# Performance work log

Measured on AMD Instinct MI355X. Metric: run time of the kernel, lower is better.

Reference implementation:

```python
import jax, jax.numpy as jnp
import numpy as np

NUM_GROUPS = 32
EPS = 1e-6


def group_norm(x, gamma, beta):
    # x: [b, c, h, w]
    b, c, h, w = x.shape
    g = NUM_GROUPS
    xg = x.reshape(b, g, c // g, h, w)
    mean = jnp.mean(xg, axis=(2, 3, 4), keepdims=True)
    var = jnp.var(xg, axis=(2, 3, 4), keepdims=True)
    xg = (xg - mean) * jax.lax.rsqrt(var + EPS)
    x = xg.reshape(b, c, h, w)
    return x * gamma[None, :, None, None] + beta[None, :, None, None]


def conv1x1(x, w, bias):
    # x: [b, c_in, h, w], w: [c_out, c_in], bias: [c_out]
    return jnp.einsum('bihw,oi->bohw', x, w) + bias[None, :, None, None]


def setup_inputs() -> dict:
    key = jax.random.key(0)
    ks = jax.random.split(key, 10)
    c = 512
    b, h, w = 4, 64, 64
    scale = 1.0 / np.sqrt(c)
    inp = {
        'x': jax.random.normal(ks[0], (b, c, h, w), dtype=jnp.float32),
        'gn_gamma': jnp.ones((c,), dtype=jnp.float32),
        'gn_beta': jnp.zeros((c,), dtype=jnp.float32),
        'wq': jax.random.normal(ks[1], (c, c), dtype=jnp.float32) * scale,
        'bq': jnp.zeros((c,), dtype=jnp.float32),
        'wk': jax.random.normal(ks[2], (c, c), dtype=jnp.float32) * scale,
        'bk': jnp.zeros((c,), dtype=jnp.float32),
        'wv': jax.random.normal(ks[3], (c, c), dtype=jnp.float32) * scale,
        'bv': jnp.zeros((c,), dtype=jnp.float32),
        'wo': jax.random.normal(ks[4], (c, c), dtype=jnp.float32) * scale,
        'bo': jnp.zeros((c,), dtype=jnp.float32),
    }
    return inp


def reference(x, gn_gamma, gn_beta, wq, bq, wk, bk, wv, bv, wo, bo):
    b, c, h, w = x.shape
    h_ = group_norm(x, gn_gamma, gn_beta)
    q = conv1x1(h_, wq, bq)
    k = conv1x1(h_, wk, bk)
    v = conv1x1(h_, wv, bv)
    n = h * w
    q = q.reshape(b, c, n).transpose(0, 2, 1)  # [b, n, c]
    k = k.reshape(b, c, n)                      # [b, c, n]
    v = v.reshape(b, c, n).transpose(0, 2, 1)  # [b, n, c]
    sim = jnp.einsum('bqc,bck->bqk', q, k) * (c ** -0.5)  # [b, n, n]
    attn = jax.nn.softmax(sim, axis=-1)
    out = jnp.einsum('bqk,bkc->bqc', attn, v)  # [b, n, c]
    out = out.transpose(0, 2, 1).reshape(b, c, h, w)
    out = conv1x1(out, wo, bo)
    return x + out
```

## Files before the change

### kernel.cpp

```cpp
#include <hip/hip_runtime.h>


typedef __attribute__((ext_vector_type(8))) short bf16x8;
typedef __attribute__((ext_vector_type(4))) float f32x4;

#define MFMA16(a, b, c) __builtin_amdgcn_mfma_f32_16x16x32_bf16((a), (b), (c), 0, 0, 0)

#define B_   4
#define C_   512
#define N_   4096
#define SCALE 0.044194173824159216f
#define ESHIFT 12.0f

__device__ __forceinline__ unsigned short f2bf(float f) {
    union { float f; unsigned int u; } v; v.f = f;
    unsigned int r = (v.u + 0x7fffu + ((v.u >> 16) & 1u)) >> 16;
    return (unsigned short)r;
}
__device__ __forceinline__ float bf2f(unsigned short s) {
    union { unsigned int u; float f; } v; v.u = ((unsigned int)s) << 16;
    return v.f;
}

__device__ __forceinline__ void async16(const unsigned short* g, unsigned short* l) {
    __builtin_amdgcn_global_load_lds((const __attribute__((address_space(1))) unsigned int*)g,
                                     (__attribute__((address_space(3))) unsigned int*)l,
                                     16, 0, 0);
}

__global__ __launch_bounds__(256) void gn_partial(const float* __restrict__ x,
                                                  float* __restrict__ part) {
    int blk = blockIdx.x;
    int gid = blk >> 2, qtr = blk & 3;
    const float4* base = (const float4*)(x + (size_t)gid * 65536) + qtr * 4096;
    float s = 0.f, ss = 0.f;
    for (int i = threadIdx.x; i < 4096; i += 256) {
        float4 v = base[i];
        s  += v.x + v.y + v.z + v.w;
        ss += v.x * v.x + v.y * v.y + v.z * v.z + v.w * v.w;
    }
    __shared__ float red[512];
    int t = threadIdx.x;
    red[t] = s; red[256 + t] = ss;
    __syncthreads();
    for (int st = 128; st > 0; st >>= 1) {
        if (t < st) { red[t] += red[t + st]; red[256 + t] += red[256 + t + st]; }
        __syncthreads();
    }
    if (t == 0) { part[blk] = red[0]; part[512 + blk] = red[256]; }
}

__global__ __launch_bounds__(256) void gn_apply(const float* __restrict__ x,
                                                const float* __restrict__ gamma,
                                                const float* __restrict__ beta,
                                                const float* __restrict__ part,
                                                unsigned short* __restrict__ ht) {
    __shared__ float tile[64][65];
    __shared__ float mrs[4][2];
    int j0 = blockIdx.x * 64, c0 = blockIdx.y * 64, b = blockIdx.z;
    int t = threadIdx.x;
    if (t < 4) {
        int gid = b * 32 + (c0 >> 4) + t;
        float s = 0.f, ss = 0.f;
#pragma unroll
        for (int q = 0; q < 4; ++q) { s += part[gid * 4 + q]; ss += part[512 + gid * 4 + q]; }
        float mean = s * (1.f / 65536.f);
        float var  = ss * (1.f / 65536.f) - mean * mean;
        mrs[t][0] = mean;
        mrs[t][1] = rsqrtf(var + 1e-6f);
    }
    __syncthreads();
#pragma unroll
    for (int i = 0; i < 16; ++i) {
        int lid = i * 256 + t;
        int cl = lid >> 6, jl = lid & 63;
        int c = c0 + cl;
        float v = x[((size_t)b * C_ + c) * N_ + j0 + jl];
        tile[cl][jl] = (v - mrs[cl >> 4][0]) * mrs[cl >> 4][1] * gamma[c] + beta[c];
    }
    __syncthreads();
#pragma unroll
    for (int i = 0; i < 16; ++i) {
        int lid = i * 256 + t;
        int jl = lid >> 6, cl = lid & 63;
        ht[((size_t)b * N_ + j0 + jl) * C_ + c0 + cl] = f2bf(tile[cl][jl]);
    }
}

__global__ __launch_bounds__(256) void wconv(const float* __restrict__ wq,
                                             const float* __restrict__ wk,
                                             const float* __restrict__ wv,
                                             const float* __restrict__ wo,
                                             unsigned short* __restrict__ dst) {
    size_t i = (size_t)blockIdx.x * 256 + threadIdx.x;
    int m = (int)(i >> 18);
    size_t off = i & 262143;
    const float* src = (m == 0) ? wq : (m == 1) ? wk : (m == 2) ? wv : wo;
    dst[i] = f2bf(src[off]);
}

template <typename EPI>
__device__ __forceinline__ void gemm_core(const unsigned short* __restrict__ Abase,
                                          const unsigned short* __restrict__ Bbase,
                                          size_t lda, size_t ldb, int K, EPI epi) {
    __shared__ unsigned short hl[2][128 * 64];
    __shared__ unsigned short wl[2][128 * 64];
    int t = threadIdx.x;
    int wv = t >> 6, lane = t & 63, l15 = lane & 15, quad = lane >> 4;
    int wm = wv & 1, wn = wv >> 1;
    int srow = lane >> 3;
    int sch  = ((lane & 7) ^ srow) * 8;
    int xr = l15 & 7;
    f32x4 acc[4][4] = {};
#pragma unroll
    for (int i = 0; i < 4; ++i) {
        int seg = wv * 4 + i;
        size_t row = seg * 8 + srow;
        async16(&Abase[row * lda + sch], &hl[0][seg * 512]);
        async16(&Bbase[row * ldb + sch], &wl[0][seg * 512]);
    }
    int nk = K >> 6;
    for (int k = 0; k < nk; ++k) {
        int cur = k & 1;
        __builtin_amdgcn_s_waitcnt(0x3F70);
        __syncthreads();
        if (k + 1 < nk) {
            int k0 = (k + 1) << 6;
#pragma unroll
            for (int i = 0; i < 4; ++i) {
                int seg = wv * 4 + i;
                size_t row = seg * 8 + srow;
                async16(&Abase[row * lda + k0 + sch], &hl[cur ^ 1][seg * 512]);
                async16(&Bbase[row * ldb + k0 + sch], &wl[cur ^ 1][seg * 512]);
            }
        }
#pragma unroll
        for (int kk = 0; kk < 2; ++kk) {
            int sl = (((kk << 2) + quad) ^ xr) * 8;
            bf16x8 af[4], bfr[4];
#pragma unroll
            for (int mi = 0; mi < 4; ++mi)
                af[mi] = *(const bf16x8*)&hl[cur][(wm * 64 + mi * 16 + l15) * 64 + sl];
#pragma unroll
            for (int ni = 0; ni < 4; ++ni)
                bfr[ni] = *(const bf16x8*)&wl[cur][(wn * 64 + ni * 16 + l15) * 64 + sl];
#pragma unroll
            for (int mi = 0; mi < 4; ++mi)
#pragma unroll
                for (int ni = 0; ni < 4; ++ni)
                    acc[mi][ni] = MFMA16(af[mi], bfr[ni], acc[mi][ni]);
        }
    }
    epi(acc, wm, wn, l15, quad);
}

__global__ __launch_bounds__(256) void gemm_qkv(const unsigned short* __restrict__ Ht,
                                                const unsigned short* __restrict__ Wb,
                                                const float* __restrict__ bq,
                                                const float* __restrict__ bk,
                                                const float* __restrict__ bv,
                                                unsigned short* __restrict__ Qt,
                                                unsigned short* __restrict__ Kt,
                                                unsigned short* __restrict__ Vg) {
    int b = blockIdx.z, j0 = blockIdx.x * 128;
    int ct = blockIdx.y;
    int slab = ct >> 2, co0 = (ct & 3) * 128;
    const unsigned short* A = Ht + ((size_t)b * N_ + j0) * C_;
    const unsigned short* B = Wb + (size_t)slab * C_ * C_ + (size_t)co0 * C_;
    const float* bias = (slab == 0) ? bq : (slab == 1) ? bk : bv;
    unsigned short* outqk = (slab == 0) ? Qt : Kt;
    gemm_core(A, B, C_, C_, C_,
        [&](f32x4 (&acc)[4][4], int wm, int wn, int l15, int quad) {
        if (slab < 2) {
#pragma unroll
            for (int mi = 0; mi < 4; ++mi)
#pragma unroll
                for (int ni = 0; ni < 4; ++ni)
#pragma unroll
                    for (int r = 0; r < 4; ++r) {
                        int mrow = wm * 64 + mi * 16 + quad * 4 + r;
                        int ncol = wn * 64 + ni * 16 + l15;
                        outqk[((size_t)b * N_ + j0 + mrow) * C_ + co0 + ncol] =
                            f2bf(acc[mi][ni][r] + bias[co0 + ncol]);
                    }
        } else {
#pragma unroll
            for (int mi = 0; mi < 4; ++mi)
#pragma unroll
                for (int ni = 0; ni < 4; ++ni) {
                    int ncol = wn * 64 + ni * 16 + l15;
                    float bb = bias[co0 + ncol];
                    ushort4 pk;
                    pk.x = f2bf(acc[mi][ni][0] + bb);
                    pk.y = f2bf(acc[mi][ni][1] + bb);
                    pk.z = f2bf(acc[mi][ni][2] + bb);
                    pk.w = f2bf(acc[mi][ni][3] + bb);
                    int jb = j0 + wm * 64 + mi * 16 + quad * 4;
                    *(ushort4*)&Vg[((size_t)b * C_ + co0 + ncol) * N_ + jb] = pk;
                }
        }
    });
}

__global__ __launch_bounds__(512, 2) void gemm_qk_exp(const unsigned short* __restrict__ Qt,
                                                      const unsigned short* __restrict__ Kt,
                                                      unsigned short* __restrict__ P,
                                                      float* __restrict__ psum) {
    extern __shared__ unsigned short sm[];
    int b = blockIdx.z, j0 = blockIdx.x * 256, ky = blockIdx.y;
    int kc0 = ky * 256;
    const unsigned short* A  = Qt + ((size_t)b * N_ + j0) * C_;
    const unsigned short* Bm = Kt + ((size_t)b * N_ + kc0) * C_;

    int t = threadIdx.x;
    int w = t >> 6, lane = t & 63, l15 = lane & 15, quad = lane >> 4;
    int wm = w >> 2, wn = w & 3;
    int srow = lane >> 2;
    int sch  = (((lane & 3) ^ ((lane >> 3) & 3))) * 8;
    int slotq = (quad ^ ((l15 >> 1) & 3)) * 8;

    f32x4 acc[8][4] = {};

    const int NT = 16;
#pragma unroll
    for (int tt = 0; tt < 3; ++tt) {
        unsigned short* dst = sm + (tt << 14);
        size_t k0 = (size_t)tt << 5;
#pragma unroll
        for (int i = 0; i < 2; ++i) {
            int seg = w * 2 + i;
            size_t row = (size_t)seg * 16 + srow;
            async16(&A [row * C_ + k0 + sch], dst + seg * 512);
            async16(&Bm[row * C_ + k0 + sch], dst + 8192 + seg * 512);
        }
    }
    __builtin_amdgcn_s_waitcnt(0x3F78);
    __builtin_amdgcn_s_barrier();

    for (int tt = 0; tt < NT; ++tt) {
        const unsigned short* bp = sm + ((tt & 3) << 14);
        unsigned short* stg = sm + (((tt + 3) & 3) << 14);
        const bool dostage = (tt + 3 < NT);
        size_t k0n = (size_t)(tt + 3) << 5;
        bf16x8 bfr[4], af[4];
#pragma unroll
        for (int ni = 0; ni < 4; ++ni)
            bfr[ni] = *(const bf16x8*)&bp[8192 + (wn * 64 + ni * 16 + l15) * 32 + slotq];
#pragma unroll
        for (int mi = 0; mi < 4; ++mi)
            af[mi] = *(const bf16x8*)&bp[(wm * 128 + mi * 16 + l15) * 32 + slotq];
        if (dostage) {
#pragma unroll
            for (int i = 0; i < 2; ++i) {
                int seg = w * 2 + i;
                size_t row = (size_t)seg * 16 + srow;
                async16(&A[row * C_ + k0n + sch], stg + seg * 512);
            }
        }
        __builtin_amdgcn_s_barrier();
        __builtin_amdgcn_s_setprio(1);
#pragma unroll
        for (int mi = 0; mi < 4; ++mi)
#pragma unroll
            for (int ni = 0; ni < 4; ++ni)
                acc[mi][ni] = MFMA16(af[mi], bfr[ni], acc[mi][ni]);
        __builtin_amdgcn_s_setprio(0);
        __builtin_amdgcn_s_barrier();
#pragma unroll
        for (int mi = 0; mi < 4; ++mi)
            af[mi] = *(const bf16x8*)&bp[(wm * 128 + (mi + 4) * 16 + l15) * 32 + slotq];
        if (dostage) {
#pragma unroll
            for (int i = 0; i < 2; ++i) {
                int seg = w * 2 + i;
                size_t row = (size_t)seg * 16 + srow;
                async16(&Bm[row * C_ + k0n + sch], stg + 8192 + seg * 512);
            }
        }
        __builtin_amdgcn_s_barrier();
        __builtin_amdgcn_s_setprio(1);
#pragma unroll
        for (int mi = 0; mi < 4; ++mi)
#pragma unroll
            for (int ni = 0; ni < 4; ++ni)
                acc[4 + mi][ni] = MFMA16(af[mi], bfr[ni], acc[4 + mi][ni]);
        __builtin_amdgcn_s_setprio(0);
        if (tt + 1 < NT) {
            if (tt < NT - 3)       __builtin_amdgcn_s_waitcnt(0x3F78);
            else if (tt == NT - 3) __builtin_amdgcn_s_waitcnt(0x3F74);
            else                   __builtin_amdgcn_s_waitcnt(0x3F70);
            __builtin_amdgcn_s_barrier();
        }
    }

#pragma unroll
    for (int mi = 0; mi < 8; ++mi) {
        float rs[4] = {0.f, 0.f, 0.f, 0.f};
#pragma unroll
        for (int ni = 0; ni < 4; ++ni) {
            int ncol = kc0 + wn * 64 + ni * 16 + l15;
#pragma unroll
            for (int r = 0; r < 4; ++r) {
                int mrow = j0 + wm * 128 + mi * 16 + quad * 4 + r;
                float p = __expf(acc[mi][ni][r] * SCALE - ESHIFT);
                rs[r] += p;
                P[((size_t)b * N_ + mrow) * N_ + ncol] = f2bf(p);
            }
        }
#pragma unroll
        for (int r = 0; r < 4; ++r) {
            float v = rs[r];
            v += __shfl_xor(v, 1);
            v += __shfl_xor(v, 2);
            v += __shfl_xor(v, 4);
            v += __shfl_xor(v, 8);
            if (l15 == 0)
                psum[(size_t)(wn * 16 + ky) * 16384 +
                     (size_t)b * N_ + j0 + wm * 128 + mi * 16 + quad * 4 + r] = v;
        }
    }
}

__global__ __launch_bounds__(256) void gemm_pv(const unsigned short* __restrict__ P,
                                               const unsigned short* __restrict__ Vg,
                                               const float* __restrict__ psum,
                                               unsigned short* __restrict__ ao) {
    __shared__ float linv[128];
    int flat = blockIdx.x;
    int xcd = flat & 7, rr = flat >> 3;
    int ct = rr & 3, g = (rr >> 2) * 8 + xcd;
    int b = g & 3, qtile = g >> 2;
    int j0 = qtile * 128, co0 = ct * 128;
    int t = threadIdx.x;
    if (t < 128) {
        size_t q = (size_t)b * N_ + j0 + t;
        float s = 0.f;
#pragma unroll
        for (int i = 0; i < 64; ++i) s += psum[(size_t)i * 16384 + q];
        linv[t] = 1.f / s;
    }
    const unsigned short* A = P + ((size_t)b * N_ + j0) * N_;
    const unsigned short* B = Vg + ((size_t)b * C_ + co0) * N_;
    gemm_core(A, B, N_, N_, N_,
        [&](f32x4 (&acc)[4][4], int wm, int wn, int l15, int quad) {
#pragma unroll
        for (int mi = 0; mi < 4; ++mi)
#pragma unroll
            for (int ni = 0; ni < 4; ++ni)
#pragma unroll
                for (int r = 0; r < 4; ++r) {
                    int mrow = wm * 64 + mi * 16 + quad * 4 + r;
                    int ncol = wn * 64 + ni * 16 + l15;
                    ao[((size_t)b * N_ + j0 + mrow) * C_ + co0 + ncol] =
                        f2bf(acc[mi][ni][r] * linv[mrow]);
                }
    });
}

__global__ __launch_bounds__(256) void gemm_resid(const unsigned short* __restrict__ AObf,
                                                  const unsigned short* __restrict__ Wo,
                                                  const float* __restrict__ bo,
                                                  const float* __restrict__ xres,
                                                  float* __restrict__ out) {
    int b = blockIdx.z, j0 = blockIdx.x * 128, co0 = blockIdx.y * 128;
    const unsigned short* A = AObf + ((size_t)b * N_ + j0) * C_;
    const unsigned short* B = Wo + (size_t)co0 * C_;
    gemm_core(A, B, C_, C_, C_,
        [&](f32x4 (&acc)[4][4], int wm, int wn, int l15, int quad) {
#pragma unroll
        for (int mi = 0; mi < 4; ++mi)
#pragma unroll
            for (int ni = 0; ni < 4; ++ni) {
                int ncol = wn * 64 + ni * 16 + l15;
                int jb = j0 + wm * 64 + mi * 16 + quad * 4;
                size_t o = ((size_t)b * C_ + co0 + ncol) * N_ + jb;
                float bb = bo[co0 + ncol];
                float4 xr = *(const float4*)&xres[o];
                float4 ov;
                ov.x = acc[mi][ni][0] + bb + xr.x;
                ov.y = acc[mi][ni][1] + bb + xr.y;
                ov.z = acc[mi][ni][2] + bb + xr.z;
                ov.w = acc[mi][ni][3] + bb + xr.w;
                *(float4*)&out[o] = ov;
            }
    });
}

__global__ __launch_bounds__(256, 1) void flash_attn(const unsigned short* __restrict__ Qt,
                                                     const unsigned short* __restrict__ Kt,
                                                     const unsigned short* __restrict__ Vg,
                                                     unsigned short* __restrict__ part,
                                                     float* __restrict__ lbuf,
                                                     int nsplit) {
    extern __shared__ unsigned short smem[];
    unsigned short* Kl = smem;
    unsigned short* Vl = smem + 32768;
    unsigned short* Pl = smem + 65536;

    int flat = blockIdx.x;
    int qblk, b, s;
    if (nsplit == 2) { s = flat & 1; b = (flat >> 1) & 3; qblk = flat >> 3; }
    else             { s = 0;        b = flat & 3;        qblk = flat >> 2; }
    int q0 = qblk * 128;
    int t = threadIdx.x, w = t >> 6, lane = t & 63, l15 = lane & 15, quad = lane >> 4;
    int klen = N_ / nsplit, kbeg = s * klen, nkt = klen / 32;
    int xr = l15 & 7;

    const unsigned short* Kbase = Kt + (size_t)b * N_ * C_;
    const unsigned short* Vbase = Vg + (size_t)b * C_ * N_;

    bf16x8 qa[2][16];
#pragma unroll
    for (int u = 0; u < 2; ++u) {
        const unsigned short* qb =
            Qt + ((size_t)b * N_ + q0 + w * 32 + u * 16 + l15) * C_ + quad * 8;
#pragma unroll
        for (int ck = 0; ck < 16; ++ck) qa[u][ck] = *(const bf16x8*)(qb + ck * 32);
    }

    f32x4 o[2][32] = {};
    float lrow[2][4] = {};

    {
        int k0 = kbeg;
#pragma unroll
        for (int i = 0; i < 8; ++i) {
            int r = w * 8 + i;
            async16(Kbase + (size_t)(k0 + r) * C_ + ((lane ^ (r & 7)) * 8), Kl + r * 512);
        }
#pragma unroll
        for (int i = 0; i < 8; ++i) {
            int idx = w * 8 + i, kc = idx >> 3, cb = idx & 7;
            async16(Vbase + (size_t)(cb * 64 + lane) * N_ + k0 + kc * 8,
                    Vl + (kc * 512 + cb * 64) * 8);
        }
    }

    for (int kt = 0; kt < nkt; ++kt) {
        int cur = kt & 1, nxt = cur ^ 1;
        __builtin_amdgcn_s_waitcnt(0x3F70);
        __syncthreads();
        if (kt + 1 < nkt) {
            int k0 = kbeg + (kt + 1) * 32;
#pragma unroll
            for (int i = 0; i < 8; ++i) {
                int r = w * 8 + i;
                async16(Kbase + (size_t)(k0 + r) * C_ + ((lane ^ (r & 7)) * 8),
                        Kl + nxt * 16384 + r * 512);
            }
#pragma unroll
            for (int i = 0; i < 8; ++i) {
                int idx = w * 8 + i, kc = idx >> 3, cb = idx & 7;
                async16(Vbase + (size_t)(cb * 64 + lane) * N_ + k0 + kc * 8,
                        Vl + nxt * 16384 + (kc * 512 + cb * 64) * 8);
            }
        }
        const unsigned short* Kc = Kl + cur * 16384;
        f32x4 s00 = {}, s01 = {}, s10 = {}, s11 = {};
#pragma unroll
        for (int ck = 0; ck < 16; ++ck) {
            int slot = (ck * 4 + quad) ^ xr;
            bf16x8 b0 = *(const bf16x8*)&Kc[l15 * 512 + slot * 8];
            bf16x8 b1 = *(const bf16x8*)&Kc[(16 + l15) * 512 + slot * 8];
            s00 = MFMA16(qa[0][ck], b0, s00);
            s10 = MFMA16(qa[1][ck], b0, s10);
            s01 = MFMA16(qa[0][ck], b1, s01);
            s11 = MFMA16(qa[1][ck], b1, s11);
        }
        unsigned short* pb = &Pl[w * 1152];
#pragma unroll
        for (int r = 0; r < 4; ++r) {
            float p00 = __expf(s00[r] * SCALE - ESHIFT);
            float p01 = __expf(s01[r] * SCALE - ESHIFT);
            float p10 = __expf(s10[r] * SCALE - ESHIFT);
            float p11 = __expf(s11[r] * SCALE - ESHIFT);
            lrow[0][r] += p00 + p01;
            lrow[1][r] += p10 + p11;
            int row0 = (quad * 4 + r) * 36;
            int row1 = (16 + quad * 4 + r) * 36;
            pb[row0 + l15]      = f2bf(p00);
            pb[row0 + 16 + l15] = f2bf(p01);
            pb[row1 + l15]      = f2bf(p10);
            pb[row1 + 16 + l15] = f2bf(p11);
        }
        __builtin_amdgcn_s_waitcnt(0xC07F);
        bf16x8 pa0 = *(const bf16x8*)&Pl[w * 1152 + l15 * 36 + quad * 8];
        bf16x8 pa1 = *(const bf16x8*)&Pl[w * 1152 + (16 + l15) * 36 + quad * 8];
        const unsigned short* Vc = Vl + cur * 16384;
#pragma unroll
        for (int cf = 0; cf < 32; ++cf) {
            bf16x8 vb = *(const bf16x8*)&Vc[(quad * 512 + cf * 16 + l15) * 8];
            o[0][cf] = MFMA16(pa0, vb, o[0][cf]);
            o[1][cf] = MFMA16(pa1, vb, o[1][cf]);
        }
    }
#pragma unroll
    for (int u = 0; u < 2; ++u)
#pragma unroll
        for (int r = 0; r < 4; ++r) {
            float l = lrow[u][r];
            l += __shfl_xor(l, 1);
            l += __shfl_xor(l, 2);
            l += __shfl_xor(l, 4);
            l += __shfl_xor(l, 8);
            lrow[u][r] = l;
        }
    size_t pbase = (size_t)(s * B_ + b) * N_;
#pragma unroll
    for (int u = 0; u < 2; ++u)
#pragma unroll
        for (int cf = 0; cf < 32; ++cf)
#pragma unroll
            for (int r = 0; r < 4; ++r) {
                int q = q0 + w * 32 + u * 16 + quad * 4 + r;
                part[(pbase + q) * C_ + cf * 16 + l15] = f2bf(o[u][cf][r]);
            }
    if (l15 == 0) {
#pragma unroll
        for (int u = 0; u < 2; ++u)
#pragma unroll
            for (int r = 0; r < 4; ++r) {
                int q = q0 + w * 32 + u * 16 + quad * 4 + r;
                lbuf[pbase + q] = lrow[u][r];
            }
    }
}

__global__ __launch_bounds__(256) void attn_combine(const unsigned short* __restrict__ part,
                                                    const float* __restrict__ lbuf,
                                                    unsigned short* __restrict__ ao,
                                                    int nsplit) {
    size_t idx = (size_t)blockIdx.x * 256 + threadIdx.x;
    int cu = (int)(idx & 63);
    size_t row = idx >> 6;
    float l = lbuf[row];
    union { uint4 v; unsigned short u[8]; } p1, p2, outv;
    p1.v = *(const uint4*)&part[row * C_ + cu * 8];
    if (nsplit == 2) {
        l += lbuf[(size_t)B_ * N_ + row];
        p2.v = *(const uint4*)&part[((size_t)B_ * N_ + row) * C_ + cu * 8];
    } else {
        p2.v = make_uint4(0, 0, 0, 0);
    }
    float inv = 1.f / l;
#pragma unroll
    for (int j = 0; j < 8; ++j)
        outv.u[j] = f2bf((bf2f(p1.u[j]) + bf2f(p2.u[j])) * inv);
    *(uint4*)&ao[row * C_ + cu * 8] = outv.v;
}

extern "C" void kernel_launch(void* const* d_in, const int* in_sizes, int n_in,
                              void* d_out, int out_size, void* d_ws, size_t ws_size,
                              hipStream_t stream) {
    const float* x   = (const float*)d_in[0];
    const float* gam = (const float*)d_in[1];
    const float* bet = (const float*)d_in[2];
    const float* wq  = (const float*)d_in[3];
    const float* bq  = (const float*)d_in[4];
    const float* wk  = (const float*)d_in[5];
    const float* bk  = (const float*)d_in[6];
    const float* wv  = (const float*)d_in[7];
    const float* bv  = (const float*)d_in[8];
    const float* wo  = (const float*)d_in[9];
    const float* bo  = (const float*)d_in[10];
    float* out = (float*)d_out;

    char* ws = (char*)d_ws;
    const size_t SZH = (size_t)B_ * N_ * C_ * 2;
    const size_t OFF_HT = 4096;
    const size_t OFF_QT = OFF_HT + SZH;
    const size_t OFF_KT = OFF_QT + SZH;
    const size_t OFF_VG = OFF_KT + SZH;
    const size_t OFF_WB = OFF_VG + SZH;
    const size_t OFF_X  = OFF_WB + 2097152;
    float*          part0 = (float*)ws;
    unsigned short* Ht    = (unsigned short*)(ws + OFF_HT);
    unsigned short* Qt    = (unsigned short*)(ws + OFF_QT);
    unsigned short* Kt    = (unsigned short*)(ws + OFF_KT);
    unsigned short* Vg    = (unsigned short*)(ws + OFF_VG);
    unsigned short* Wb    = (unsigned short*)(ws + OFF_WB);
    unsigned short* AObf  = Ht;

    const size_t SZPSUM = 64ull * 16384 * 4;
    const size_t SZP    = (size_t)B_ * N_ * N_ * 2;
    float*          psum = (float*)(ws + OFF_X);
    unsigned short* P    = (unsigned short*)(ws + OFF_X + SZPSUM);
    size_t needA = OFF_X + SZPSUM + SZP;

    float*          lbuf = (float*)(ws + OFF_X);
    unsigned short* partb = (unsigned short*)(ws + OFF_X + 262144);
    size_t needB2 = OFF_X + 262144 + 2 * SZH;

    gn_partial<<<512, 256, 0, stream>>>(x, part0);
    gn_apply<<<dim3(64, 8, B_), 256, 0, stream>>>(x, gam, bet, part0, Ht);
    wconv<<<4096, 256, 0, stream>>>(wq, wk, wv, wo, Wb);
    gemm_qkv<<<dim3(32, 12, B_), 256, 0, stream>>>(Ht, Wb, bq, bk, bv, Qt, Kt, Vg);

    if (ws_size >= needA) {
        const int QK_LDS = 131072;
        (void)hipFuncSetAttribute((const void*)gemm_qk_exp,
                                  hipFuncAttributeMaxDynamicSharedMemorySize, QK_LDS);
        gemm_qk_exp<<<dim3(16, 16, B_), 512, QK_LDS, stream>>>(Qt, Kt, P, psum);
        gemm_pv<<<512, 256, 0, stream>>>(P, Vg, psum, AObf);
    } else {
        int nsplit = (ws_size >= needB2) ? 2 : 1;
        const int FLASH_LDS = 140288;
        (void)hipFuncSetAttribute((const void*)flash_attn,
                                  hipFuncAttributeMaxDynamicSharedMemorySize, FLASH_LDS);
        flash_attn<<<dim3(32 * B_ * nsplit), 256, FLASH_LDS, stream>>>(Qt, Kt, Vg, partb, lbuf, nsplit);
        attn_combine<<<4096, 256, 0, stream>>>(partb, lbuf, AObf, nsplit);
    }
    gemm_resid<<<dim3(32, 4, B_), 256, 0, stream>>>(AObf, Wb + 786432, bo, x, out);
}
```

Measured before the change: 352.4 us.

## Enlarge PV GEMM tile to 256 rows with 4-stage async pipeline and remap QK blocks

```diff
diff --git a/kernel.cpp b/kernel.cpp
--- a/kernel.cpp
+++ b/kernel.cpp
@@ -207,7 +207,14 @@
                                                       unsigned short* __restrict__ P,
                                                       float* __restrict__ psum) {
     extern __shared__ unsigned short sm[];
-    int b = blockIdx.z, j0 = blockIdx.x * 256, ky = blockIdx.y;
+    int lin = blockIdx.x + 16 * blockIdx.y + 256 * blockIdx.z;
+    int xcd = lin & 7;
+    int i4  = lin >> 3;
+    int idx = i4 & 31;
+    int b   = i4 >> 5;
+    int rq  = xcd & 3, rk = xcd >> 2;
+    int j0  = (rq * 4 + (idx & 3)) * 256;
+    int ky  = rk * 8 + (idx >> 2);
     int kc0 = ky * 256;
     const unsigned short* A  = Qt + ((size_t)b * N_ + j0) * C_;
     const unsigned short* Bm = Kt + ((size_t)b * N_ + kc0) * C_;
@@ -321,40 +328,102 @@
     }
 }
 
-__global__ __launch_bounds__(256) void gemm_pv(const unsigned short* __restrict__ P,
-                                               const unsigned short* __restrict__ Vg,
-                                               const float* __restrict__ psum,
-                                               unsigned short* __restrict__ ao) {
-    __shared__ float linv[128];
-    int flat = blockIdx.x;
-    int xcd = flat & 7, rr = flat >> 3;
-    int ct = rr & 3, g = (rr >> 2) * 8 + xcd;
-    int b = g & 3, qtile = g >> 2;
-    int j0 = qtile * 128, co0 = ct * 128;
+__global__ __launch_bounds__(512, 2) void gemm_pv(const unsigned short* __restrict__ P,
+                                                  const unsigned short* __restrict__ Vg,
+                                                  const float* __restrict__ psum,
+                                                  unsigned short* __restrict__ ao) {
+    extern __shared__ unsigned short sm[];
+    __shared__ float linv[256];
+    int lin = blockIdx.x;
+    int xcd = lin & 7;
+    int i4  = lin >> 3;
+    int ct  = i4 & 3;
+    int grp = xcd + 8 * (i4 >> 2);
+    int b = grp & 3, qtile = grp >> 2;
+    int j0 = qtile * 256, co0 = ct * 128;
     int t = threadIdx.x;
-    if (t < 128) {
+    int w = t >> 6, lane = t & 63, l15 = lane & 15, quad = lane >> 4;
+    int wm = w >> 1, wn = w & 1;
+    int srow = lane >> 2;
+    int sch  = ((lane & 3) ^ ((lane >> 3) & 3)) * 8;
+    int slotq = (quad ^ ((l15 >> 1) & 3)) * 8;
+    const unsigned short* A  = P  + ((size_t)b * N_ + j0) * N_;
+    const unsigned short* Bm = Vg + ((size_t)b * C_ + co0) * N_;
+    f32x4 acc[4][4] = {};
+    const int NT = 128;
+#pragma unroll
+    for (int tt = 0; tt < 3; ++tt) {
+        unsigned short* dst = sm + tt * 12288;
+        size_t k0 = (size_t)tt << 5;
+#pragma unroll
+        for (int i = 0; i < 2; ++i) {
+            int seg = w * 2 + i;
+            size_t row = (size_t)seg * 16 + srow;
+            async16(&A[row * N_ + k0 + sch], dst + seg * 512);
+        }
+        {
+            size_t row = (size_t)w * 16 + srow;
+            async16(&Bm[row * N_ + k0 + sch], dst + 8192 + w * 512);
+        }
+    }
+    if (t < 256) {
         size_t q = (size_t)b * N_ + j0 + t;
         float s = 0.f;
 #pragma unroll
         for (int i = 0; i < 64; ++i) s += psum[(size_t)i * 16384 + q];
         linv[t] = 1.f / s;
     }
-    const unsigned short* A = P + ((size_t)b * N_ + j0) * N_;
-    const unsigned short* B = Vg + ((size_t)b * C_ + co0) * N_;
-    gemm_core(A, B, N_, N_, N_,
-        [&](f32x4 (&acc)[4][4], int wm, int wn, int l15, int quad) {
+    __builtin_amdgcn_s_waitcnt(0x3F76);
+    __builtin_amdgcn_s_barrier();
+    for (int tt = 0; tt < NT; ++tt) {
+        const unsigned short* bp = sm + (tt & 3) * 12288;
+        bf16x8 af[4], bfr[4];
 #pragma unroll
         for (int mi = 0; mi < 4; ++mi)
+            af[mi] = *(const bf16x8*)&bp[(wm * 64 + mi * 16 + l15) * 32 + slotq];
+#pragma unroll
+        for (int ni = 0; ni < 4; ++ni)
+            bfr[ni] = *(const bf16x8*)&bp[8192 + (wn * 64 + ni * 16 + l15) * 32 + slotq];
+        if (tt + 3 < NT) {
+            unsigned short* stg = sm + ((tt + 3) & 3) * 12288;
+            size_t k0n = (size_t)(tt + 3) << 5;
+#pragma unroll
+            for (int i = 0; i < 2; ++i) {
+                int seg = w * 2 + i;
+                size_t row = (size_t)seg * 16 + srow;
+                async16(&A[row * N_ + k0n + sch], stg + seg * 512);
+            }
+            {
+                size_t row = (size_t)w * 16 + srow;
+                async16(&Bm[row * N_ + k0n + sch], stg + 8192 + w * 512);
+            }
+        }
+        __builtin_amdgcn_s_barrier();
+        __builtin_amdgcn_s_setprio(1);
+#pragma unroll
+        for (int mi = 0; mi < 4; ++mi)
 #pragma unroll
             for (int ni = 0; ni < 4; ++ni)
-#pragma unroll
-                for (int r = 0; r < 4; ++r) {
-                    int mrow = wm * 64 + mi * 16 + quad * 4 + r;
-                    int ncol = wn * 64 + ni * 16 + l15;
-                    ao[((size_t)b * N_ + j0 + mrow) * C_ + co0 + ncol] =
-                        f2bf(acc[mi][ni][r] * linv[mrow]);
-                }
-    });
+                acc[mi][ni] = MFMA16(af[mi], bfr[ni], acc[mi][ni]);
+        __builtin_amdgcn_s_setprio(0);
+        if (tt + 1 < NT) {
+            if (tt + 3 < NT)      __builtin_amdgcn_s_waitcnt(0x3F76);
+            else if (tt + 2 < NT) __builtin_amdgcn_s_waitcnt(0x3F73);
+            else                  __builtin_amdgcn_s_waitcnt(0x3F70);
+            __builtin_amdgcn_s_barrier();
+        }
+    }
+#pragma unroll
+    for (int mi = 0; mi < 4; ++mi)
+#pragma unroll
+        for (int ni = 0; ni < 4; ++ni)
+#pragma unroll
+            for (int r = 0; r < 4; ++r) {
+                int mrow = wm * 64 + mi * 16 + quad * 4 + r;
+                int ncol = wn * 64 + ni * 16 + l15;
+                ao[((size_t)b * N_ + j0 + mrow) * C_ + co0 + ncol] =
+                    f2bf(acc[mi][ni][r] * linv[mrow]);
+            }
 }
 
 __global__ __launch_bounds__(256) void gemm_resid(const unsigned short* __restrict__ AObf,
@@ -601,7 +670,10 @@
         (void)hipFuncSetAttribute((const void*)gemm_qk_exp,
                                   hipFuncAttributeMaxDynamicSharedMemorySize, QK_LDS);
         gemm_qk_exp<<<dim3(16, 16, B_), 512, QK_LDS, stream>>>(Qt, Kt, P, psum);
-        gemm_pv<<<512, 256, 0, stream>>>(P, Vg, psum, AObf);
+        const int PV_LDS = 98304;
+        (void)hipFuncSetAttribute((const void*)gemm_pv,
+                                  hipFuncAttributeMaxDynamicSharedMemorySize, PV_LDS);
+        gemm_pv<<<256, 512, PV_LDS, stream>>>(P, Vg, psum, AObf);
     } else {
         int nsplit = (ws_size >= needB2) ? 2 : 1;
         const int FLASH_LDS = 140288;
```

Measured after the change: 341.8 us. 1.03x faster.
